# Performance work log

Hardware: AMD Instinct MI355X
Metric: run time of the kernel (lower is better)

The kernel has to match this reference:

```python
import jax, jax.numpy as jnp
import numpy as np

BN_EPS = 1e-5

def _pair_indices(f0, f1):
    row, col = [], []
    for i in range(f0):
        for j in range(i + 1, f1):
            row.append(i); col.append(j)
    return np.asarray(row, np.int32), np.asarray(col, np.int32)

def setup_inputs() -> dict:
    key = jax.random.key(0)
    ks = jax.random.split(key, 6)
    B, F0, F1, E = 4096, 32, 32, 32
    I = F0 * (F0 - 1) // 2  # 496 pairs for F0 == F1
    xi = jax.random.normal(ks[0], (B, F0, E), jnp.float32)
    xj = jax.random.normal(ks[1], (B, F1, E), jnp.float32)
    # xavier_uniform over (1, I, E): bound = sqrt(6/(I+E)) approximated by normal scale
    W = jax.random.normal(ks[2], (1, I, E), jnp.float32) * np.sqrt(2.0 / (I + E))
    bn_gamma = jnp.ones((I,), jnp.float32)
    bn_beta = jnp.zeros((I,), jnp.float32)
    attn_w = jax.random.normal(ks[3], (E, E), jnp.float32) / np.sqrt(E)
    attn_b = jnp.zeros((E,), jnp.float32)
    proj_w = jax.random.normal(ks[4], (E, 1), jnp.float32) / np.sqrt(E)
    proj_b = jnp.zeros((1,), jnp.float32)
    return {"xi": xi, "xj": xj, "W": W, "bn_gamma": bn_gamma, "bn_beta": bn_beta,
            "attn_w": attn_w, "attn_b": attn_b, "proj_w": proj_w, "proj_b": proj_b}

def reference(xi, xj, W, bn_gamma, bn_beta, attn_w, attn_b, proj_w, proj_b):
    f0, f1 = xi.shape[1], xj.shape[1]
    row, col = _pair_indices(f0, f1)
    p = xi[:, row, :]              # [B, I, E]
    q = xj[:, col, :]              # [B, I, E]
    out = p * q
    # BatchNorm1d(I) on [B, I, E] in training mode: stats over (batch, emb)
    mean = jnp.mean(out, axis=(0, 2), keepdims=True)
    var = jnp.mean(jnp.square(out - mean), axis=(0, 2), keepdims=True)
    out = (out - mean) * jax.lax.rsqrt(var + BN_EPS)
    out = out * bn_gamma[None, :, None] + bn_beta[None, :, None]
    out = out * W                   # broadcast [1, I, E]
    # attention: linear -> relu -> linear -> softmax over interaction dim
    h = jax.nn.relu(jnp.einsum('bie,ea->bia', out, attn_w) + attn_b)
    logits = jnp.einsum('bia,ao->bio', h, proj_w) + proj_b  # [B, I, 1]
    scores = jax.nn.softmax(logits, axis=1)
    return scores * out
```

## Files before the change

### kernel.cpp

```cpp
#include <hip/hip_runtime.h>

#define NB 4096
#define F0 32
#define F1 32
#define NE 32
#define NI 496
#define BN_EPS 1e-5f
#define XPAD 36

typedef float f32x4_t __attribute__((ext_vector_type(4)));

__device__ __forceinline__ void pair_rc_loop(int i, int& r, int& c) {
    int rem = i, rr = 0;
    while (rem >= F1 - 1 - rr) { rem -= F1 - 1 - rr; ++rr; }
    r = rr; c = rr + 1 + rem;
}

__device__ __forceinline__ void pair_rc_fast(int i, int& r, int& c) {
    int rr = (int)((63.0f - sqrtf(3969.0f - 8.0f * (float)i)) * 0.5f);
    int off = rr * (63 - rr) / 2;
    if (off > i) { --rr; off = rr * (63 - rr) / 2; }
    else {
        int off2 = (rr + 1) * (62 - rr) / 2;
        if (off2 <= i) { rr = rr + 1; off = off2; }
    }
    r = rr; c = rr + 1 + (i - off);
}

__global__ __launch_bounds__(256) void stats_kernel(
        const float* __restrict__ xi, const float* __restrict__ xj,
        const float* __restrict__ gamma, const float* __restrict__ beta,
        float* __restrict__ scale, float* __restrict__ shift) {
    const int i = blockIdx.x;
    int r, c; pair_rc_loop(i, r, c);
    const int t  = threadIdx.x;
    const int e4 = t & 7;
    const int bs = t >> 3;

    const float4* xi4 = (const float4*)xi;
    const float4* xj4 = (const float4*)xj;

    float4 s1 = {0.f,0.f,0.f,0.f};
    float4 s2 = {0.f,0.f,0.f,0.f};
    for (int b = bs; b < NB; b += 32) {
        float4 a = xi4[(b*F0 + r)*8 + e4];
        float4 q = xj4[(b*F1 + c)*8 + e4];
        float x0 = a.x*q.x, x1 = a.y*q.y, x2 = a.z*q.z, x3 = a.w*q.w;
        s1.x += x0; s1.y += x1; s1.z += x2; s1.w += x3;
        s2.x += x0*x0; s2.y += x1*x1; s2.z += x2*x2; s2.w += x3*x3;
    }
    float p1 = (s1.x + s1.y) + (s1.z + s1.w);
    float p2 = (s2.x + s2.y) + (s2.z + s2.w);
    for (int off = 32; off; off >>= 1) {
        p1 += __shfl_down(p1, off);
        p2 += __shfl_down(p2, off);
    }
    __shared__ float r1[4], r2[4];
    const int wv = t >> 6;
    if ((t & 63) == 0) { r1[wv] = p1; r2[wv] = p2; }
    __syncthreads();
    if (t == 0) {
        float S1 = (r1[0] + r1[1]) + (r1[2] + r1[3]);
        float S2 = (r2[0] + r2[1]) + (r2[2] + r2[3]);
        const float invN = 1.0f / (float)(NB * NE);
        float mean = S1 * invN;
        float var  = S2 * invN - mean * mean;
        float sc   = gamma[i] / sqrtf(var + BN_EPS);
        scale[i] = sc;
        shift[i] = beta[i] - mean * sc;
    }
}

__global__ __launch_bounds__(256) void main_kernel(
        const float* __restrict__ xi, const float* __restrict__ xj,
        const float* __restrict__ W,
        const float* __restrict__ attn_w, const float* __restrict__ attn_b,
        const float* __restrict__ proj_w, const float* __restrict__ proj_b,
        const float* __restrict__ scale, const float* __restrict__ shift,
        float* __restrict__ out) {
    __shared__ __attribute__((aligned(16))) float xi_l[F0 * XPAD];
    __shared__ __attribute__((aligned(16))) float xj_l[F1 * XPAD];
    __shared__ float ss_l[NI * 2];
    __shared__ float lg[NI];
    __shared__ int   rc_l[NI];
    __shared__ float redm[4], reds[4];

    const int b = blockIdx.x;
    const int t = threadIdx.x;

    {
        const float4* x4 = (const float4*)(xi + (size_t)b * F0 * NE);
        const float4* y4 = (const float4*)(xj + (size_t)b * F1 * NE);
        const int r  = t >> 3;
        const int e0 = (t & 7) * 4;
        *(float4*)&xi_l[r * XPAD + e0] = x4[t];
        *(float4*)&xj_l[r * XPAD + e0] = y4[t];
        for (int s = t; s < NI; s += 256) {
            ss_l[2*s]   = scale[s];
            ss_l[2*s+1] = shift[s];
        }
    }
    __syncthreads();

    const float4* W4  = (const float4*)W;
    const float4* aw4 = (const float4*)attn_w;
    const float4* ab4 = (const float4*)attn_b;
    const float4* pw4 = (const float4*)proj_w;
    const float  pb   = proj_b[0];

    #pragma unroll
    for (int round = 0; round < 2; ++round) {
        const int i = t + round * 256;
        if (i < NI) {
            int r, c; pair_rc_fast(i, r, c);
            rc_l[i] = (r << 5) | c;
            const float sc = ss_l[2*i], sh = ss_l[2*i+1];
            const float4* xir = (const float4*)&xi_l[r * XPAD];
            const float4* xjc = (const float4*)&xj_l[c * XPAD];

            float4 h[8];
            #pragma unroll
            for (int a4 = 0; a4 < 8; ++a4) h[a4] = ab4[a4];

            #pragma unroll
            for (int g = 0; g < 8; ++g) {
                const float4 av = xir[g];
                const float4 qv = xjc[g];
                const float4 wv = W4[i*8 + g];
                float og[4];
                og[0] = wv.x * (sc * av.x * qv.x + sh);
                og[1] = wv.y * (sc * av.y * qv.y + sh);
                og[2] = wv.z * (sc * av.z * qv.z + sh);
                og[3] = wv.w * (sc * av.w * qv.w + sh);
                #pragma unroll
                for (int k = 0; k < 4; ++k) {
                    const float s = og[k];
                    const int e = 4*g + k;
                    #pragma unroll
                    for (int a4 = 0; a4 < 8; ++a4) {
                        const float4 wr = aw4[e*8 + a4];
                        h[a4].x += s * wr.x;
                        h[a4].y += s * wr.y;
                        h[a4].z += s * wr.z;
                        h[a4].w += s * wr.w;
                    }
                }
            }

            float logit = pb;
            #pragma unroll
            for (int a4 = 0; a4 < 8; ++a4) {
                const float4 pw = pw4[a4];
                logit += fmaxf(h[a4].x, 0.f) * pw.x + fmaxf(h[a4].y, 0.f) * pw.y
                       + fmaxf(h[a4].z, 0.f) * pw.z + fmaxf(h[a4].w, 0.f) * pw.w;
            }
            lg[i] = logit;
        }
    }
    __syncthreads();

    float m = -1e30f;
    for (int f = t; f < NI; f += 256) m = fmaxf(m, lg[f]);
    for (int off = 32; off; off >>= 1) m = fmaxf(m, __shfl_xor(m, off));
    const int wv = t >> 6;
    if ((t & 63) == 0) redm[wv] = m;
    __syncthreads();
    m = fmaxf(fmaxf(redm[0], redm[1]), fmaxf(redm[2], redm[3]));

    float s = 0.f;
    for (int f = t; f < NI; f += 256) s += expf(lg[f] - m);
    for (int off = 32; off; off >>= 1) s += __shfl_xor(s, off);
    if ((t & 63) == 0) reds[wv] = s;
    __syncthreads();
    const float inv = 1.0f / ((reds[0] + reds[1]) + (reds[2] + reds[3]));

    for (int f = t; f < NI; f += 256) lg[f] = expf(lg[f] - m) * inv;
    __syncthreads();

    f32x4_t* op4 = (f32x4_t*)(out + (size_t)b * NI * NE);
    for (int f4 = t; f4 < NI * 8; f4 += 256) {
        const int i  = f4 >> 3;
        const int e0 = (f4 & 7) * 4;
        const int rc = rc_l[i];
        const int r  = rc >> 5, c = rc & 31;
        const float sc = ss_l[2*i], sh = ss_l[2*i+1];
        const float score = lg[i];
        const float4 w = W4[f4];
        f32x4_t res;
        res.x = score * (w.x * (sc * xi_l[r*XPAD+e0+0] * xj_l[c*XPAD+e0+0] + sh));
        res.y = score * (w.y * (sc * xi_l[r*XPAD+e0+1] * xj_l[c*XPAD+e0+1] + sh));
        res.z = score * (w.z * (sc * xi_l[r*XPAD+e0+2] * xj_l[c*XPAD+e0+2] + sh));
        res.w = score * (w.w * (sc * xi_l[r*XPAD+e0+3] * xj_l[c*XPAD+e0+3] + sh));
        __builtin_nontemporal_store(res, &op4[f4]);
    }
}

extern "C" void kernel_launch(void* const* d_in, const int* in_sizes, int n_in,
                              void* d_out, int out_size, void* d_ws, size_t ws_size,
                              hipStream_t stream) {
    const float* xi     = (const float*)d_in[0];
    const float* xj     = (const float*)d_in[1];
    const float* W      = (const float*)d_in[2];
    const float* gamma  = (const float*)d_in[3];
    const float* beta   = (const float*)d_in[4];
    const float* attn_w = (const float*)d_in[5];
    const float* attn_b = (const float*)d_in[6];
    const float* proj_w = (const float*)d_in[7];
    const float* proj_b = (const float*)d_in[8];
    float* out = (float*)d_out;

    float* scale = (float*)d_ws;
    float* shift = scale + NI;

    stats_kernel<<<NI, 256, 0, stream>>>(xi, xj, gamma, beta, scale, shift);
    main_kernel<<<NB, 256, 0, stream>>>(xi, xj, W, attn_w, attn_b,
                                        proj_w, proj_b, scale, shift, out);
}
```

Before: 144.8 us.

## Restructure BN stats as batch-tiled all-pairs partials plus a reduction kernel

The per-pair stats kernel, which re-read xi/xj rows from global memory once for every pair, is replaced by a two-stage scheme. In the first stage each block stages 8 batches in shared memory and accumulates sum and sum-of-squares for all 32x32 row/col combinations, writing partials to workspace. A small second kernel reduces the partials and computes scale and shift for the valid upper-triangle pairs. This removes redundant global reads at the cost of an extra launch, workspace traffic and work on unused lower-triangle pairs. The main kernel also preloads W into registers and caches the softmax exponentials so expf is computed once per logit.

```diff
diff --git a/kernel.cpp b/kernel.cpp
--- a/kernel.cpp
+++ b/kernel.cpp
@@ -1,20 +1,17 @@
 #include <hip/hip_runtime.h>
 
 #define NB 4096
-#define F0 32
-#define F1 32
+#define NF 32
 #define NE 32
 #define NI 496
 #define BN_EPS 1e-5f
 #define XPAD 36
 
+#define SA_BLOCKS 512
+#define SA_BPB    8
+#define SA_CHUNK  4
+
 typedef float f32x4_t __attribute__((ext_vector_type(4)));
-
-__device__ __forceinline__ void pair_rc_loop(int i, int& r, int& c) {
-    int rem = i, rr = 0;
-    while (rem >= F1 - 1 - rr) { rem -= F1 - 1 - rr; ++rr; }
-    r = rr; c = rr + 1 + rem;
-}
 
 __device__ __forceinline__ void pair_rc_fast(int i, int& r, int& c) {
     int rr = (int)((63.0f - sqrtf(3969.0f - 8.0f * (float)i)) * 0.5f);
@@ -27,47 +24,92 @@
     r = rr; c = rr + 1 + (i - off);
 }
 
-__global__ __launch_bounds__(256) void stats_kernel(
+__global__ __launch_bounds__(256) void statsA(
         const float* __restrict__ xi, const float* __restrict__ xj,
+        float* __restrict__ part) {
+    __shared__ __attribute__((aligned(16))) float xi_l[SA_CHUNK * NF * XPAD];
+    __shared__ __attribute__((aligned(16))) float xj_l[SA_CHUNK * NF * XPAD];
+    const int t  = threadIdx.x;
+    const int r  = t >> 3;
+    const int cg = t & 7;
+
+    float4 acc1[4] = {{0,0,0,0},{0,0,0,0},{0,0,0,0},{0,0,0,0}};
+    float4 acc2[4] = {{0,0,0,0},{0,0,0,0},{0,0,0,0},{0,0,0,0}};
+
+    for (int ch = 0; ch < SA_BPB / SA_CHUNK; ++ch) {
+        const int b0 = blockIdx.x * SA_BPB + ch * SA_CHUNK;
+        const float4* xs = (const float4*)(xi + (size_t)b0 * NF * NE);
+        const float4* ys = (const float4*)(xj + (size_t)b0 * NF * NE);
+        if (ch) __syncthreads();
+        #pragma unroll
+        for (int k = 0; k < 4; ++k) {
+            const int idx = t + 256 * k;
+            const int row = idx >> 3;
+            const int e4  = idx & 7;
+            *(float4*)&xi_l[row * XPAD + e4 * 4] = xs[idx];
+            *(float4*)&xj_l[row * XPAD + e4 * 4] = ys[idx];
+        }
+        __syncthreads();
+        #pragma unroll
+        for (int bb = 0; bb < SA_CHUNK; ++bb) {
+            const float* xr  = &xi_l[(bb * NF + r) * XPAD];
+            const float* xc0 = &xj_l[(bb * NF) * XPAD];
+            #pragma unroll
+            for (int e4 = 0; e4 < 8; ++e4) {
+                const float4 av = *(const float4*)&xr[e4 * 4];
+                #pragma unroll
+                for (int k = 0; k < 4; ++k) {
+                    const int c = cg + 8 * k;
+                    const float4 qv = *(const float4*)&xc0[c * XPAD + e4 * 4];
+                    float px = av.x * qv.x, py = av.y * qv.y;
+                    float pz = av.z * qv.z, pw = av.w * qv.w;
+                    acc1[k].x += px; acc1[k].y += py;
+                    acc1[k].z += pz; acc1[k].w += pw;
+                    acc2[k].x += px * px; acc2[k].y += py * py;
+                    acc2[k].z += pz * pz; acc2[k].w += pw * pw;
+                }
+            }
+        }
+    }
+
+    float* dst = part + (size_t)blockIdx.x * 2048;
+    #pragma unroll
+    for (int k = 0; k < 4; ++k) {
+        const int c = cg + 8 * k;
+        const int j = r * 32 + c;
+        float g1 = (acc1[k].x + acc1[k].y) + (acc1[k].z + acc1[k].w);
+        float g2 = (acc2[k].x + acc2[k].y) + (acc2[k].z + acc2[k].w);
+        *(float2*)&dst[2 * j] = make_float2(g1, g2);
+    }
+}
+
+__global__ __launch_bounds__(256) void statsB(
+        const float* __restrict__ part,
         const float* __restrict__ gamma, const float* __restrict__ beta,
         float* __restrict__ scale, float* __restrict__ shift) {
-    const int i = blockIdx.x;
-    int r, c; pair_rc_loop(i, r, c);
-    const int t  = threadIdx.x;
-    const int e4 = t & 7;
-    const int bs = t >> 3;
-
-    const float4* xi4 = (const float4*)xi;
-    const float4* xj4 = (const float4*)xj;
-
-    float4 s1 = {0.f,0.f,0.f,0.f};
-    float4 s2 = {0.f,0.f,0.f,0.f};
-    for (int b = bs; b < NB; b += 32) {
-        float4 a = xi4[(b*F0 + r)*8 + e4];
-        float4 q = xj4[(b*F1 + c)*8 + e4];
-        float x0 = a.x*q.x, x1 = a.y*q.y, x2 = a.z*q.z, x3 = a.w*q.w;
-        s1.x += x0; s1.y += x1; s1.z += x2; s1.w += x3;
-        s2.x += x0*x0; s2.y += x1*x1; s2.z += x2*x2; s2.w += x3*x3;
-    }
-    float p1 = (s1.x + s1.y) + (s1.z + s1.w);
-    float p2 = (s2.x + s2.y) + (s2.z + s2.w);
-    for (int off = 32; off; off >>= 1) {
-        p1 += __shfl_down(p1, off);
-        p2 += __shfl_down(p2, off);
-    }
-    __shared__ float r1[4], r2[4];
-    const int wv = t >> 6;
-    if ((t & 63) == 0) { r1[wv] = p1; r2[wv] = p2; }
-    __syncthreads();
-    if (t == 0) {
-        float S1 = (r1[0] + r1[1]) + (r1[2] + r1[3]);
-        float S2 = (r2[0] + r2[1]) + (r2[2] + r2[3]);
-        const float invN = 1.0f / (float)(NB * NE);
-        float mean = S1 * invN;
-        float var  = S2 * invN - mean * mean;
-        float sc   = gamma[i] / sqrtf(var + BN_EPS);
-        scale[i] = sc;
-        shift[i] = beta[i] - mean * sc;
+    __shared__ float sums[256];
+    const int t = threadIdx.x;
+    const int base = blockIdx.x * 256;
+    float s = 0.f;
+    #pragma unroll 4
+    for (int p = 0; p < SA_BLOCKS; ++p)
+        s += part[(size_t)p * 2048 + base + t];
+    sums[t] = s;
+    __syncthreads();
+    if (t < 128) {
+        const int q = blockIdx.x * 128 + t;
+        const int r = q >> 5, c = q & 31;
+        if (c > r) {
+            const float g1 = sums[2 * t];
+            const float g2 = sums[2 * t + 1];
+            const float invN = 1.0f / (float)(NB * NE);
+            const float mean = g1 * invN;
+            const float var  = g2 * invN - mean * mean;
+            const int   i    = r * (63 - r) / 2 + (c - r - 1);
+            const float sc   = gamma[i] / sqrtf(var + BN_EPS);
+            scale[i] = sc;
+            shift[i] = beta[i] - mean * sc;
+        }
     }
 }
 
@@ -78,8 +120,8 @@
         const float* __restrict__ proj_w, const float* __restrict__ proj_b,
         const float* __restrict__ scale, const float* __restrict__ shift,
         float* __restrict__ out) {
-    __shared__ __attribute__((aligned(16))) float xi_l[F0 * XPAD];
-    __shared__ __attribute__((aligned(16))) float xj_l[F1 * XPAD];
+    __shared__ __attribute__((aligned(16))) float xi_l[NF * XPAD];
+    __shared__ __attribute__((aligned(16))) float xj_l[NF * XPAD];
     __shared__ float ss_l[NI * 2];
     __shared__ float lg[NI];
     __shared__ int   rc_l[NI];
@@ -89,8 +131,8 @@
     const int t = threadIdx.x;
 
     {
-        const float4* x4 = (const float4*)(xi + (size_t)b * F0 * NE);
-        const float4* y4 = (const float4*)(xj + (size_t)b * F1 * NE);
+        const float4* x4 = (const float4*)(xi + (size_t)b * NF * NE);
+        const float4* y4 = (const float4*)(xj + (size_t)b * NF * NE);
         const int r  = t >> 3;
         const int e0 = (t & 7) * 4;
         *(float4*)&xi_l[r * XPAD + e0] = x4[t];
@@ -118,6 +160,10 @@
             const float4* xir = (const float4*)&xi_l[r * XPAD];
             const float4* xjc = (const float4*)&xj_l[c * XPAD];
 
+            float4 wv[8];
+            #pragma unroll
+            for (int g = 0; g < 8; ++g) wv[g] = W4[i*8 + g];
+
             float4 h[8];
             #pragma unroll
             for (int a4 = 0; a4 < 8; ++a4) h[a4] = ab4[a4];
@@ -126,12 +172,11 @@
             for (int g = 0; g < 8; ++g) {
                 const float4 av = xir[g];
                 const float4 qv = xjc[g];
-                const float4 wv = W4[i*8 + g];
                 float og[4];
-                og[0] = wv.x * (sc * av.x * qv.x + sh);
-                og[1] = wv.y * (sc * av.y * qv.y + sh);
-                og[2] = wv.z * (sc * av.z * qv.z + sh);
-                og[3] = wv.w * (sc * av.w * qv.w + sh);
+                og[0] = wv[g].x * (sc * av.x * qv.x + sh);
+                og[1] = wv[g].y * (sc * av.y * qv.y + sh);
+                og[2] = wv[g].z * (sc * av.z * qv.z + sh);
+                og[3] = wv[g].w * (sc * av.w * qv.w + sh);
                 #pragma unroll
                 for (int k = 0; k < 4; ++k) {
                     const float s = og[k];
@@ -162,19 +207,23 @@
     float m = -1e30f;
     for (int f = t; f < NI; f += 256) m = fmaxf(m, lg[f]);
     for (int off = 32; off; off >>= 1) m = fmaxf(m, __shfl_xor(m, off));
-    const int wv = t >> 6;
-    if ((t & 63) == 0) redm[wv] = m;
+    const int wv_ = t >> 6;
+    if ((t & 63) == 0) redm[wv_] = m;
     __syncthreads();
     m = fmaxf(fmaxf(redm[0], redm[1]), fmaxf(redm[2], redm[3]));
 
     float s = 0.f;
-    for (int f = t; f < NI; f += 256) s += expf(lg[f] - m);
+    for (int f = t; f < NI; f += 256) {
+        const float e = expf(lg[f] - m);
+        lg[f] = e;
+        s += e;
+    }
     for (int off = 32; off; off >>= 1) s += __shfl_xor(s, off);
-    if ((t & 63) == 0) reds[wv] = s;
+    if ((t & 63) == 0) reds[wv_] = s;
     __syncthreads();
     const float inv = 1.0f / ((reds[0] + reds[1]) + (reds[2] + reds[3]));
 
-    for (int f = t; f < NI; f += 256) lg[f] = expf(lg[f] - m) * inv;
+    for (int f = t; f < NI; f += 256) lg[f] *= inv;
     __syncthreads();
 
     f32x4_t* op4 = (f32x4_t*)(out + (size_t)b * NI * NE);
@@ -209,10 +258,12 @@
     const float* proj_b = (const float*)d_in[8];
     float* out = (float*)d_out;
 
-    float* scale = (float*)d_ws;
-    float* shift = scale + NI;
-
-    stats_kernel<<<NI, 256, 0, stream>>>(xi, xj, gamma, beta, scale, shift);
+    float* part  = (float*)d_ws;
+    float* scale = part + (size_t)SA_BLOCKS * 2048;
+    float* shift = scale + 512;
+
+    statsA<<<SA_BLOCKS, 256, 0, stream>>>(xi, xj, part);
+    statsB<<<8, 256, 0, stream>>>(part, gamma, beta, scale, shift);
     main_kernel<<<NB, 256, 0, stream>>>(xi, xj, W, attn_w, attn_b,
                                         proj_w, proj_b, scale, shift, out);
 }
```

Result: slower. 160.6 us (+11.0%).
